# Performance work log

Measured on AMD Instinct MI355X. Metric: run time of the kernel, lower is better.

## Reference

```python
import jax, jax.numpy as jnp
import numpy as np

L, D, H, R = 8, 1024, 16, 16
HD = D // H  # head dim


def setup_inputs() -> dict:
    key = jax.random.key(0)
    ks = jax.random.split(key, 7)
    s = 0.02  # init scale for stability
    return {
        "x": jax.random.normal(ks[0], (2, 1024, D), jnp.float32),
        "Wqkv": jax.random.normal(ks[1], (L, D, 3 * D), jnp.float32) * s,
        "Aqkv": jax.random.normal(ks[2], (L, D, R), jnp.float32) * s,
        "Bqkv": jax.random.normal(ks[3], (L, R, 3 * D), jnp.float32) * s,
        "Wproj": jax.random.normal(ks[4], (L, D, D), jnp.float32) * s,
        "Aproj": jax.random.normal(ks[5], (L, D, R), jnp.float32) * s,
        "Bproj": jax.random.normal(ks[6], (L, R, D), jnp.float32) * s,
    }


def _forward(x, Wqkv, Aqkv, Bqkv, Wproj, Aproj, Bproj):
    B, S, _ = x.shape
    # causal mask [S, S]
    mask = jnp.tril(jnp.ones((S, S), bool))

    def layer(h, p):
        Wq, Aq, Bq, Wp, Ap, Bp = p
        # LoRA merge exactly as the module: p + A @ B, then dense matmul
        Wq_m = Wq + Aq @ Bq            # [D, 3D]
        Wp_m = Wp + Ap @ Bp            # [D, D]
        qkv = h @ Wq_m                 # [B, S, 3D]
        q, k, v = jnp.split(qkv, 3, axis=-1)
        q = q.reshape(B, S, H, HD).transpose(0, 2, 1, 3)  # [B,H,S,hd]
        k = k.reshape(B, S, H, HD).transpose(0, 2, 1, 3)
        v = v.reshape(B, S, H, HD).transpose(0, 2, 1, 3)
        scores = jnp.einsum("bhqd,bhkd->bhqk", q, k) / np.sqrt(HD)
        scores = jnp.where(mask, scores, jnp.finfo(scores.dtype).min)
        attn = jax.nn.softmax(scores, axis=-1)
        o = jnp.einsum("bhqk,bhkd->bhqd", attn, v)        # [B,H,S,hd]
        o = o.transpose(0, 2, 1, 3).reshape(B, S, D)
        return h + o @ Wp_m, None

    out, _ = jax.lax.scan(layer, x, (Wqkv, Aqkv, Bqkv, Wproj, Aproj, Bproj))
    return out


def reference(x, Wqkv, Aqkv, Bqkv, Wproj, Aproj, Bproj):
    return _forward(x, Wqkv, Aqkv, Bqkv, Wproj, Aproj, Bproj)
```

## Files before the change

### kernel.cpp

```cpp
#include <hip/hip_runtime.h>
#include <hip/hip_bf16.h>


typedef unsigned short ushort_t;
typedef __attribute__((ext_vector_type(8))) short bf16x8;
typedef __attribute__((ext_vector_type(4))) float f32x4;

__device__ __forceinline__ unsigned short f2bf(float f) {
    union { float f; unsigned int u; } x; x.f = f;
    unsigned int r = x.u + 0x7fffu + ((x.u >> 16) & 1u);
    return (unsigned short)(r >> 16);
}

__device__ __forceinline__ f32x4 mfma16(bf16x8 a, bf16x8 b, f32x4 c) {
    return __builtin_amdgcn_mfma_f32_16x16x32_bf16(a, b, c, 0, 0, 0);
}

typedef const __attribute__((address_space(1))) unsigned int* gas_ptr;
typedef __attribute__((address_space(3))) unsigned int* las_ptr;
__device__ __forceinline__ void lds_stage16(const void* g, void* l) {
    __builtin_amdgcn_global_load_lds((gas_ptr)(unsigned long long)g,
                                     (las_ptr)(unsigned int)(unsigned long long)l,
                                     16, 0, 0);
}

#define RORMAX(x, C)                                                           \
    x = fmaxf(x, __int_as_float(__builtin_amdgcn_mov_dpp(                      \
                     __float_as_int(x), C, 0xf, 0xf, false)));
#define RORADD(x, C)                                                           \
    x += __int_as_float(__builtin_amdgcn_mov_dpp(                              \
        __float_as_int(x), C, 0xf, 0xf, false));

__global__ __launch_bounds__(256) void convert_x(
    const float4* __restrict__ in, float4* __restrict__ outF,
    ushort4* __restrict__ outB, int n4) {
    int i = blockIdx.x * 256 + threadIdx.x;
    if (i < n4) {
        float4 v = in[i];
        outF[i] = v;
        ushort4 o;
        o.x = f2bf(v.x); o.y = f2bf(v.y); o.z = f2bf(v.z); o.w = f2bf(v.w);
        outB[i] = o;
    }
}

__global__ __launch_bounds__(256) void merge_T(
    const float* __restrict__ W, const float* __restrict__ A,
    const float* __restrict__ Bm, unsigned short* __restrict__ WT, int N) {
    __shared__ float t[32][132];
    __shared__ float Asl[32][17];
    const int z = blockIdx.z;
    W  += (size_t)z * 1024 * N;
    A  += (size_t)z * 1024 * 16;
    Bm += (size_t)z * 16 * N;
    WT += (size_t)z * N * 1024;
    int j0 = blockIdx.x * 128, i0 = blockIdx.y * 32;
    int tx = threadIdx.x & 31, ty = threadIdx.x >> 5;

    if (threadIdx.x < 128) {
        int r = threadIdx.x >> 2, c4 = (threadIdx.x & 3) * 4;
        float4 a = *(const float4*)&A[(size_t)(i0 + r) * 16 + c4];
        Asl[r][c4 + 0] = a.x; Asl[r][c4 + 1] = a.y;
        Asl[r][c4 + 2] = a.z; Asl[r][c4 + 3] = a.w;
    }
    float4 bv[16];
    #pragma unroll
    for (int r = 0; r < 16; r++)
        bv[r] = *(const float4*)&Bm[(size_t)r * N + j0 + tx * 4];
    float4 wv[4];
    #pragma unroll
    for (int ii0 = 0; ii0 < 4; ii0++)
        wv[ii0] = *(const float4*)&W[(size_t)(i0 + ty + ii0 * 8) * N + j0 + tx * 4];
    __syncthreads();

    #pragma unroll
    for (int ii0 = 0; ii0 < 4; ii0++) {
        int ii = ty + ii0 * 8;
        float4 acc = wv[ii0];
        #pragma unroll
        for (int r = 0; r < 16; r++) {
            float a = Asl[ii][r];
            acc.x += a * bv[r].x; acc.y += a * bv[r].y;
            acc.z += a * bv[r].z; acc.w += a * bv[r].w;
        }
        *(float4*)&t[ii][tx * 4] = acc;
    }
    __syncthreads();
    int jj = threadIdx.x >> 1, half = threadIdx.x & 1;
    bf16x8 o0, o1;
    #pragma unroll
    for (int c = 0; c < 8; c++) o0[c] = (short)f2bf(t[half * 16 + c][jj]);
    #pragma unroll
    for (int c = 0; c < 8; c++) o1[c] = (short)f2bf(t[half * 16 + 8 + c][jj]);
    unsigned short* dst = &WT[(size_t)(j0 + jj) * 1024 + i0 + half * 16];
    *(bf16x8*)dst = o0;
    *(bf16x8*)(dst + 8) = o1;
}

__global__ __launch_bounds__(256) void gemm_bf16_128(
    const unsigned short* __restrict__ A,
    const unsigned short* __restrict__ BT,
    unsigned short* __restrict__ outB,
    int M, int N, int K, int scaleq) {
    __shared__ __align__(16) unsigned short As[2][128 * 32];
    __shared__ __align__(16) unsigned short Bs[2][128 * 32];
    const int tid = threadIdx.x;
    const int m0 = blockIdx.y * 128, n0 = blockIdx.x * 128;
    const int w = tid >> 6, lane = tid & 63;
    const int wm = (w >> 1) * 64, wn = (w & 1) * 64;
    const int lr = lane & 15, quad = lane >> 4;
    const int srow = w * 16 + (lane >> 2);
    const int skof = (lane & 3) * 8;

    f32x4 acc[4][4] = {};

    for (int k0 = 0; k0 < K; k0 += 64) {
        __syncthreads();
        #pragma unroll
        for (int h = 0; h < 2; h++) {
            lds_stage16(A  + (size_t)(m0 + srow)      * K + k0 + h * 32 + skof,
                        (char*)As[h] + w * 1024);
            lds_stage16(A  + (size_t)(m0 + 64 + srow) * K + k0 + h * 32 + skof,
                        (char*)As[h] + 4096 + w * 1024);
            lds_stage16(BT + (size_t)(n0 + srow)      * K + k0 + h * 32 + skof,
                        (char*)Bs[h] + w * 1024);
            lds_stage16(BT + (size_t)(n0 + 64 + srow) * K + k0 + h * 32 + skof,
                        (char*)Bs[h] + 4096 + w * 1024);
        }
        __syncthreads();

        #pragma unroll
        for (int h = 0; h < 2; h++) {
            bf16x8 af[4], bfr[4];
            #pragma unroll
            for (int i = 0; i < 4; i++) {
                af[i]  = *(const bf16x8*)&As[h][(wm + i * 16 + lr) * 32 + quad * 8];
                bfr[i] = *(const bf16x8*)&Bs[h][(wn + i * 16 + lr) * 32 + quad * 8];
            }
            #pragma unroll
            for (int i = 0; i < 4; i++)
                #pragma unroll
                for (int j = 0; j < 4; j++)
                    acc[i][j] = mfma16(af[i], bfr[j], acc[i][j]);
        }
    }
    #pragma unroll
    for (int i = 0; i < 4; i++)
        #pragma unroll
        for (int j = 0; j < 4; j++)
            #pragma unroll
            for (int r = 0; r < 4; r++) {
                int row = m0 + wm + i * 16 + quad * 4 + r;
                int col = n0 + wn + j * 16 + lr;
                float v = acc[i][j][r];
                if (scaleq && col < 1024) v *= 0.125f;
                outB[(size_t)row * N + col] = f2bf(v);
            }
}

__global__ __launch_bounds__(256) void gemm_bf16_64(
    const unsigned short* __restrict__ A,
    const unsigned short* __restrict__ BT,
    const float* __restrict__ res,
    float* __restrict__ outF,
    unsigned short* __restrict__ outB,
    int M, int N, int K) {
    __shared__ __align__(16) unsigned short As[2][64 * 32];
    __shared__ __align__(16) unsigned short Bs[2][64 * 32];
    const int tid = threadIdx.x;
    const int m0 = blockIdx.y * 64, n0 = blockIdx.x * 64;
    const int w = tid >> 6, lane = tid & 63;
    const int wm = (w >> 1) * 32, wn = (w & 1) * 32;
    const int lr = lane & 15, quad = lane >> 4;
    const int srow = w * 16 + (lane >> 2);
    const int skof = (lane & 3) * 8;

    f32x4 acc[2][2] = {};

    for (int k0 = 0; k0 < K; k0 += 64) {
        __syncthreads();
        #pragma unroll
        for (int h = 0; h < 2; h++) {
            lds_stage16(A  + (size_t)(m0 + srow) * K + k0 + h * 32 + skof,
                        (char*)As[h] + w * 1024);
            lds_stage16(BT + (size_t)(n0 + srow) * K + k0 + h * 32 + skof,
                        (char*)Bs[h] + w * 1024);
        }
        __syncthreads();

        #pragma unroll
        for (int h = 0; h < 2; h++) {
            bf16x8 af[2], bfr[2];
            #pragma unroll
            for (int i = 0; i < 2; i++) {
                af[i]  = *(const bf16x8*)&As[h][(wm + i * 16 + lr) * 32 + quad * 8];
                bfr[i] = *(const bf16x8*)&Bs[h][(wn + i * 16 + lr) * 32 + quad * 8];
            }
            #pragma unroll
            for (int i = 0; i < 2; i++)
                #pragma unroll
                for (int j = 0; j < 2; j++)
                    acc[i][j] = mfma16(af[i], bfr[j], acc[i][j]);
        }
    }
    #pragma unroll
    for (int i = 0; i < 2; i++)
        #pragma unroll
        for (int j = 0; j < 2; j++)
            #pragma unroll
            for (int r = 0; r < 4; r++) {
                int row = m0 + wm + i * 16 + quad * 4 + r;
                int col = n0 + wn + j * 16 + lr;
                float v = acc[i][j][r] + res[(size_t)row * N + col];
                if (outF) outF[(size_t)row * N + col] = v;
                if (outB) outB[(size_t)row * N + col] = f2bf(v);
            }
}

__global__ __launch_bounds__(256) void vtrans(
    const unsigned short* __restrict__ qkv, unsigned short* __restrict__ VT) {
    __shared__ unsigned short t[32][33];
    int bh = blockIdx.z, b = bh >> 4, h = bh & 15;
    int s0 = blockIdx.x * 32, d0 = blockIdx.y * 32;
    int tx = threadIdx.x & 31, ty = threadIdx.x >> 5;
    for (int i = ty; i < 32; i += 8)
        t[i][tx] = qkv[(size_t)(b * 1024 + s0 + i) * 3072 + 2048 + h * 64 + d0 + tx];
    __syncthreads();
    for (int i = ty; i < 32; i += 8)
        VT[((size_t)bh * 64 + d0 + i) * 1024 + s0 + tx] = t[tx][i];
}

__global__ __launch_bounds__(256) void attn_kernel(
    const unsigned short* __restrict__ qkv,
    const unsigned short* __restrict__ VT,
    unsigned short* __restrict__ O) {
    __shared__ __align__(16) unsigned short Ks[2][64 * 32];
    __shared__ __align__(16) unsigned short Vs[2][64 * 32];
    __shared__ __align__(16) unsigned short pl[4][16 * 72];
    const int tid = threadIdx.x;
    const int w = tid >> 6, lane = tid & 63;
    const int lr = lane & 15, quad = lane >> 4;
    const int bh = blockIdx.y, b = bh >> 4, h = bh & 15;
    const int qblk = (bh < 16) ? blockIdx.x : (15 - blockIdx.x);
    const int qb = qblk * 64 + w * 16;
    const int srow = w * 16 + (lane >> 2);
    const int skof = (lane & 3) * 8;
    const float LOG2E = 1.44269504f;

    const size_t rowQ = (size_t)(b * 1024 + qb + lr) * 3072 + h * 64;
    bf16x8 aq0 = *(const bf16x8*)&qkv[rowQ + quad * 8];
    bf16x8 aq1 = *(const bf16x8*)&qkv[rowQ + 32 + quad * 8];

    float m_i[4], l_i[4];
    f32x4 oacc[4] = {};
    #pragma unroll
    for (int r = 0; r < 4; r++) { m_i[r] = -1e30f; l_i[r] = 0.f; }

    const int nkt = qblk + 1;
    for (int kt64 = 0; kt64 < nkt; kt64++) {
        const int kt = kt64 << 6;
        __syncthreads();
        const size_t gK = (size_t)(b * 1024 + kt + srow) * 3072 + 1024 + h * 64;
        lds_stage16(qkv + gK + skof,      (char*)Ks[0] + w * 1024);
        lds_stage16(qkv + gK + 32 + skof, (char*)Ks[1] + w * 1024);
        const size_t gV = ((size_t)bh * 64 + srow) * 1024 + kt;
        lds_stage16(VT + gV + skof,       (char*)Vs[0] + w * 1024);
        lds_stage16(VT + gV + 32 + skof,  (char*)Vs[1] + w * 1024);
        __syncthreads();

        f32x4 s[4] = {};
        #pragma unroll
        for (int nh = 0; nh < 4; nh++) {
            bf16x8 kb0 = *(const bf16x8*)&Ks[0][(nh * 16 + lr) * 32 + quad * 8];
            bf16x8 kb1 = *(const bf16x8*)&Ks[1][(nh * 16 + lr) * 32 + quad * 8];
            s[nh] = mfma16(aq0, kb0, s[nh]);
            s[nh] = mfma16(aq1, kb1, s[nh]);
        }
        float mx[4];
        if (kt + 64 > qb) {
            #pragma unroll
            for (int r = 0; r < 4; r++) {
                int qrow = qb + quad * 4 + r;
                #pragma unroll
                for (int nh = 0; nh < 4; nh++) {
                    int kcol = kt + nh * 16 + lr;
                    s[nh][r] = (kcol <= qrow) ? s[nh][r] : -1e30f;
                }
            }
        }
        #pragma unroll
        for (int r = 0; r < 4; r++) {
            mx[r] = fmaxf(fmaxf(s[0][r], s[1][r]), fmaxf(s[2][r], s[3][r]));
            RORMAX(mx[r], 0x121) RORMAX(mx[r], 0x122)
            RORMAX(mx[r], 0x124) RORMAX(mx[r], 0x128)
        }
        float al[4];
        #pragma unroll
        for (int r = 0; r < 4; r++) {
            float mnew = fmaxf(m_i[r], mx[r]);
            al[r] = exp2f((m_i[r] - mnew) * LOG2E);
            m_i[r] = mnew;
            float lsum = 0.f;
            #pragma unroll
            for (int nh = 0; nh < 4; nh++) {
                float p = exp2f((s[nh][r] - mnew) * LOG2E);
                s[nh][r] = p;
                lsum += p;
            }
            l_i[r] = l_i[r] * al[r] + lsum;
        }
        #pragma unroll
        for (int dt = 0; dt < 4; dt++)
            #pragma unroll
            for (int r = 0; r < 4; r++) oacc[dt][r] *= al[r];
        #pragma unroll
        for (int nh = 0; nh < 4; nh++)
            #pragma unroll
            for (int r = 0; r < 4; r++)
                pl[w][(quad * 4 + r) * 72 + nh * 16 + lr] = f2bf(s[nh][r]);
        bf16x8 ap0 = *(const bf16x8*)&pl[w][lr * 72 + quad * 8];
        bf16x8 ap1 = *(const bf16x8*)&pl[w][lr * 72 + 32 + quad * 8];
        #pragma unroll
        for (int dt = 0; dt < 4; dt++) {
            bf16x8 vb0 = *(const bf16x8*)&Vs[0][(dt * 16 + lr) * 32 + quad * 8];
            bf16x8 vb1 = *(const bf16x8*)&Vs[1][(dt * 16 + lr) * 32 + quad * 8];
            oacc[dt] = mfma16(ap0, vb0, oacc[dt]);
            oacc[dt] = mfma16(ap1, vb1, oacc[dt]);
        }
    }
    #pragma unroll
    for (int r = 0; r < 4; r++) {
        RORADD(l_i[r], 0x121) RORADD(l_i[r], 0x122)
        RORADD(l_i[r], 0x124) RORADD(l_i[r], 0x128)
    }
    #pragma unroll
    for (int dt = 0; dt < 4; dt++)
        #pragma unroll
        for (int r = 0; r < 4; r++) {
            int row = b * 1024 + qb + quad * 4 + r;
            int col = h * 64 + dt * 16 + lr;
            O[(size_t)row * 1024 + col] = f2bf(oacc[dt][r] / l_i[r]);
        }
}

extern "C" void kernel_launch(void* const* d_in, const int* in_sizes, int n_in,
                              void* d_out, int out_size, void* d_ws, size_t ws_size,
                              hipStream_t stream) {
    const float* x     = (const float*)d_in[0];
    const float* Wqkv  = (const float*)d_in[1];
    const float* Aqkv  = (const float*)d_in[2];
    const float* Bqkv  = (const float*)d_in[3];
    const float* Wproj = (const float*)d_in[4];
    const float* Aproj = (const float*)d_in[5];
    const float* Bproj = (const float*)d_in[6];
    float* out = (float*)d_out;

    char* ws = (char*)d_ws;
    float* h_f32 = (float*)ws;                    ws += (size_t)2048 * 1024 * 4;
    unsigned short* h_bf   = (unsigned short*)ws; ws += (size_t)2048 * 1024 * 2;
    unsigned short* qkv_bf = (unsigned short*)ws; ws += (size_t)2048 * 3072 * 2;
    unsigned short* VT     = (unsigned short*)ws; ws += (size_t)32 * 64 * 1024 * 2;
    unsigned short* O_bf   = (unsigned short*)ws; ws += (size_t)2048 * 1024 * 2;
    unsigned short* WqT8   = (unsigned short*)ws; ws += (size_t)8 * 3072 * 1024 * 2;
    unsigned short* WpT8   = (unsigned short*)ws; ws += (size_t)8 * 1024 * 1024 * 2;

    convert_x<<<2048, 256, 0, stream>>>((const float4*)x, (float4*)h_f32,
                                        (ushort4*)h_bf, 2048 * 1024 / 4);
    merge_T<<<dim3(24, 32, 8), 256, 0, stream>>>(Wqkv, Aqkv, Bqkv, WqT8, 3072);
    merge_T<<<dim3(8, 32, 8), 256, 0, stream>>>(Wproj, Aproj, Bproj, WpT8, 1024);

    for (int l = 0; l < 8; l++) {
        const unsigned short* WqT = WqT8 + (size_t)l * 3072 * 1024;
        const unsigned short* WpT = WpT8 + (size_t)l * 1024 * 1024;
        gemm_bf16_128<<<dim3(24, 16), 256, 0, stream>>>(h_bf, WqT, qkv_bf,
                                                        2048, 3072, 1024, 1);
        vtrans<<<dim3(32, 2, 32), 256, 0, stream>>>(qkv_bf, VT);
        attn_kernel<<<dim3(16, 32), 256, 0, stream>>>(qkv_bf, VT, O_bf);
        float* outF = (l == 7) ? out : h_f32;
        gemm_bf16_64<<<dim3(16, 32), 256, 0, stream>>>(O_bf, WpT, h_f32, outF,
                                                       h_bf, 2048, 1024, 1024);
    }
}
```

Baseline: 791.6 us.

## Double-buffer LDS staging in attention and proj GEMM; fuse weight merge launches

The attention kernel and the 64x64 projection GEMM now keep two LDS buffers. The next K/V tile (or A/B tile) is issued with global_load_lds while the current tile is being computed, which removes one barrier per iteration and hides global load latency behind the MFMA work. The two LoRA merge/transpose launches are folded into a single launch of `merge_T2` that picks its weight set from the block index. The cost is twice the LDS per block, which may lower occupancy. The overlap also depends on the compiler not inserting a conservative vmcnt wait before the LDS reads.

```diff
diff --git a/kernel.cpp b/kernel.cpp
--- a/kernel.cpp
+++ b/kernel.cpp
@@ -44,17 +44,30 @@
     }
 }
 
-__global__ __launch_bounds__(256) void merge_T(
-    const float* __restrict__ W, const float* __restrict__ A,
-    const float* __restrict__ Bm, unsigned short* __restrict__ WT, int N) {
+__global__ __launch_bounds__(256) void merge_T2(
+    const float* __restrict__ Wq, const float* __restrict__ Aq,
+    const float* __restrict__ Bq, unsigned short* __restrict__ WTq,
+    const float* __restrict__ Wp, const float* __restrict__ Ap,
+    const float* __restrict__ Bp, unsigned short* __restrict__ WTp) {
     __shared__ float t[32][132];
     __shared__ float Asl[32][17];
-    const int z = blockIdx.z;
-    W  += (size_t)z * 1024 * N;
-    A  += (size_t)z * 1024 * 16;
-    Bm += (size_t)z * 16 * N;
-    WT += (size_t)z * N * 1024;
-    int j0 = blockIdx.x * 128, i0 = blockIdx.y * 32;
+    int bid = blockIdx.x;
+    const float *W, *A, *Bm;
+    unsigned short* WT;
+    int N, bx, by, bz;
+    if (bid < 6144) {
+        N = 3072; bx = bid % 24; int u = bid / 24; by = u & 31; bz = u >> 5;
+        W = Wq; A = Aq; Bm = Bq; WT = WTq;
+    } else {
+        bid -= 6144;
+        N = 1024; bx = bid & 7; int u = bid >> 3; by = u & 31; bz = u >> 5;
+        W = Wp; A = Ap; Bm = Bp; WT = WTp;
+    }
+    W  += (size_t)bz * 1024 * N;
+    A  += (size_t)bz * 1024 * 16;
+    Bm += (size_t)bz * 16 * N;
+    WT += (size_t)bz * N * 1024;
+    int j0 = bx * 128, i0 = by * 32;
     int tx = threadIdx.x & 31, ty = threadIdx.x >> 5;
 
     if (threadIdx.x < 128) {
@@ -165,8 +178,8 @@
     float* __restrict__ outF,
     unsigned short* __restrict__ outB,
     int M, int N, int K) {
-    __shared__ __align__(16) unsigned short As[2][64 * 32];
-    __shared__ __align__(16) unsigned short Bs[2][64 * 32];
+    __shared__ __align__(16) unsigned short As[2][2][64 * 32];
+    __shared__ __align__(16) unsigned short Bs[2][2][64 * 32];
     const int tid = threadIdx.x;
     const int m0 = blockIdx.y * 64, n0 = blockIdx.x * 64;
     const int w = tid >> 6, lane = tid & 63;
@@ -177,24 +190,29 @@
 
     f32x4 acc[2][2] = {};
 
-    for (int k0 = 0; k0 < K; k0 += 64) {
-        __syncthreads();
+    auto stage = [&](int k0, int buf) {
         #pragma unroll
         for (int h = 0; h < 2; h++) {
             lds_stage16(A  + (size_t)(m0 + srow) * K + k0 + h * 32 + skof,
-                        (char*)As[h] + w * 1024);
+                        (char*)As[buf][h] + w * 1024);
             lds_stage16(BT + (size_t)(n0 + srow) * K + k0 + h * 32 + skof,
-                        (char*)Bs[h] + w * 1024);
-        }
+                        (char*)Bs[buf][h] + w * 1024);
+        }
+    };
+
+    const int nk = K >> 6;
+    stage(0, 0);
+    for (int t = 0; t < nk; t++) {
         __syncthreads();
-
+        if (t + 1 < nk) stage((t + 1) << 6, (t + 1) & 1);
+        const int cur = t & 1;
         #pragma unroll
         for (int h = 0; h < 2; h++) {
             bf16x8 af[2], bfr[2];
             #pragma unroll
             for (int i = 0; i < 2; i++) {
-                af[i]  = *(const bf16x8*)&As[h][(wm + i * 16 + lr) * 32 + quad * 8];
-                bfr[i] = *(const bf16x8*)&Bs[h][(wn + i * 16 + lr) * 32 + quad * 8];
+                af[i]  = *(const bf16x8*)&As[cur][h][(wm + i * 16 + lr) * 32 + quad * 8];
+                bfr[i] = *(const bf16x8*)&Bs[cur][h][(wn + i * 16 + lr) * 32 + quad * 8];
             }
             #pragma unroll
             for (int i = 0; i < 2; i++)
@@ -234,8 +252,8 @@
     const unsigned short* __restrict__ qkv,
     const unsigned short* __restrict__ VT,
     unsigned short* __restrict__ O) {
-    __shared__ __align__(16) unsigned short Ks[2][64 * 32];
-    __shared__ __align__(16) unsigned short Vs[2][64 * 32];
+    __shared__ __align__(16) unsigned short Ks[2][2][64 * 32];
+    __shared__ __align__(16) unsigned short Vs[2][2][64 * 32];
     __shared__ __align__(16) unsigned short pl[4][16 * 72];
     const int tid = threadIdx.x;
     const int w = tid >> 6, lane = tid & 63;
@@ -256,23 +274,29 @@
     #pragma unroll
     for (int r = 0; r < 4; r++) { m_i[r] = -1e30f; l_i[r] = 0.f; }
 
+    auto stage = [&](int kt64, int buf) {
+        const int kt = kt64 << 6;
+        const size_t gK = (size_t)(b * 1024 + kt + srow) * 3072 + 1024 + h * 64;
+        lds_stage16(qkv + gK + skof,      (char*)Ks[buf][0] + w * 1024);
+        lds_stage16(qkv + gK + 32 + skof, (char*)Ks[buf][1] + w * 1024);
+        const size_t gV = ((size_t)bh * 64 + srow) * 1024 + kt;
+        lds_stage16(VT + gV + skof,       (char*)Vs[buf][0] + w * 1024);
+        lds_stage16(VT + gV + 32 + skof,  (char*)Vs[buf][1] + w * 1024);
+    };
+
     const int nkt = qblk + 1;
+    stage(0, 0);
     for (int kt64 = 0; kt64 < nkt; kt64++) {
+        __syncthreads();
+        if (kt64 + 1 < nkt) stage(kt64 + 1, (kt64 + 1) & 1);
+        const int cur = kt64 & 1;
         const int kt = kt64 << 6;
-        __syncthreads();
-        const size_t gK = (size_t)(b * 1024 + kt + srow) * 3072 + 1024 + h * 64;
-        lds_stage16(qkv + gK + skof,      (char*)Ks[0] + w * 1024);
-        lds_stage16(qkv + gK + 32 + skof, (char*)Ks[1] + w * 1024);
-        const size_t gV = ((size_t)bh * 64 + srow) * 1024 + kt;
-        lds_stage16(VT + gV + skof,       (char*)Vs[0] + w * 1024);
-        lds_stage16(VT + gV + 32 + skof,  (char*)Vs[1] + w * 1024);
-        __syncthreads();
 
         f32x4 s[4] = {};
         #pragma unroll
         for (int nh = 0; nh < 4; nh++) {
-            bf16x8 kb0 = *(const bf16x8*)&Ks[0][(nh * 16 + lr) * 32 + quad * 8];
-            bf16x8 kb1 = *(const bf16x8*)&Ks[1][(nh * 16 + lr) * 32 + quad * 8];
+            bf16x8 kb0 = *(const bf16x8*)&Ks[cur][0][(nh * 16 + lr) * 32 + quad * 8];
+            bf16x8 kb1 = *(const bf16x8*)&Ks[cur][1][(nh * 16 + lr) * 32 + quad * 8];
             s[nh] = mfma16(aq0, kb0, s[nh]);
             s[nh] = mfma16(aq1, kb1, s[nh]);
         }
@@ -322,8 +346,8 @@
         bf16x8 ap1 = *(const bf16x8*)&pl[w][lr * 72 + 32 + quad * 8];
         #pragma unroll
         for (int dt = 0; dt < 4; dt++) {
-            bf16x8 vb0 = *(const bf16x8*)&Vs[0][(dt * 16 + lr) * 32 + quad * 8];
-            bf16x8 vb1 = *(const bf16x8*)&Vs[1][(dt * 16 + lr) * 32 + quad * 8];
+            bf16x8 vb0 = *(const bf16x8*)&Vs[cur][0][(dt * 16 + lr) * 32 + quad * 8];
+            bf16x8 vb1 = *(const bf16x8*)&Vs[cur][1][(dt * 16 + lr) * 32 + quad * 8];
             oacc[dt] = mfma16(ap0, vb0, oacc[dt]);
             oacc[dt] = mfma16(ap1, vb1, oacc[dt]);
         }
@@ -366,8 +390,8 @@
 
     convert_x<<<2048, 256, 0, stream>>>((const float4*)x, (float4*)h_f32,
                                         (ushort4*)h_bf, 2048 * 1024 / 4);
-    merge_T<<<dim3(24, 32, 8), 256, 0, stream>>>(Wqkv, Aqkv, Bqkv, WqT8, 3072);
-    merge_T<<<dim3(8, 32, 8), 256, 0, stream>>>(Wproj, Aproj, Bproj, WpT8, 1024);
+    merge_T2<<<8192, 256, 0, stream>>>(Wqkv, Aqkv, Bqkv, WqT8,
+                                       Wproj, Aproj, Bproj, WpT8);
 
     for (int l = 0; l < 8; l++) {
         const unsigned short* WqT = WqT8 + (size_t)l * 3072 * 1024;
```

Result: faster. 742.3 us (-6.2%).
